# Kernel optimization log

Measured on AMD Instinct MI355X. Metric: run time of the kernel, lower is better.

## Reference

```python
import jax, jax.numpy as jnp
import numpy as np


def setup_inputs() -> dict:
    key = jax.random.key(0)
    k1, k2, k3 = jax.random.split(key, 3)
    B, T, I, H, D = 32, 1024, 1024, 16, 64
    x = jax.random.normal(k1, (B, T, I), dtype=jnp.float32)
    kv_kernel = jax.random.normal(k2, (I, H, D, 2), dtype=jnp.float32) * (1.0 / np.sqrt(I))
    q_kernel = jax.random.normal(k3, (H, D), dtype=jnp.float32) * (1.0 / np.sqrt(D))
    return {"x": x, "kv_kernel": kv_kernel, "q_kernel": q_kernel}


def _attention_rnn(x, kv_kernel, q_kernel):
    # x: [B,T,I]; kv_kernel: [I,H,D,2]; q_kernel: [H,D]
    B, T, _ = x.shape
    H, D = q_kernel.shape
    # Projection + silu activation, done once for all timesteps (same math as per-step einsum)
    kv = jnp.einsum('bti,ihdk->bthdk', x, kv_kernel)
    kv = jax.nn.silu(kv)
    k = kv[..., 0]  # [B,T,H,D]
    v = kv[..., 1]  # [B,T,H,D]
    # Per-step attention score s_t = <q_h, k_th>
    s = jnp.einsum('hd,bthd->bth', q_kernel, k)  # [B,T,H]

    # Keras RNN zero-initialized states: num [B,H,D], den [B,H], max [B,H]
    init = (
        jnp.zeros((B, H, D), x.dtype),
        jnp.zeros((B, H), x.dtype),
        jnp.zeros((B, H), x.dtype),
    )

    def step(carry, inp):
        num, den, pmax = carry
        s_t, v_t = inp  # [B,H], [B,H,D]
        cmax = jnp.maximum(pmax, s_t)
        exp_max_diff = jnp.exp(pmax - cmax)
        sm = jnp.exp(s_t - cmax)
        den_n = sm + den * exp_max_diff
        num_n = v_t * sm[..., None] + num * exp_max_diff[..., None]
        h = num_n / den_n[..., None]          # [B,H,D]
        o = jnp.sum(h, axis=-2)               # concat_heads=False -> sum over heads: [B,D]
        return (num_n, den_n, cmax), o

    # scan over time (leading axis)
    _, outs = jax.lax.scan(step, init, (jnp.swapaxes(s, 0, 1), jnp.swapaxes(v, 0, 1)))
    return jnp.swapaxes(outs, 0, 1)  # [B,T,D]


def reference(x, kv_kernel, q_kernel):
    return _attention_rnn(x, kv_kernel, q_kernel)
```

## Files before the change

### kernel.cpp

```cpp
#include <hip/hip_runtime.h>
#include <hip/hip_bf16.h>

#define B_ 32
#define T_ 1024
#define H_ 16
#define D_ 64
#define M_ (B_*T_)
#define N_ (H_*D_*2)
#define K_ 1024
#define CHUNKS 16
#define CLEN (T_/CHUNKS)

typedef __bf16 bf16x8 __attribute__((ext_vector_type(8)));
typedef float  f32x4  __attribute__((ext_vector_type(4)));
typedef unsigned short u16x8 __attribute__((ext_vector_type(8)));

__device__ __forceinline__ float bf2f(unsigned short u){
  union{ float f; unsigned int i; } c; c.i = ((unsigned int)u) << 16; return c.f;
}
__device__ __forceinline__ unsigned short f2bf(float f){
  union{ float f; unsigned int i; } c; c.f = f;
  unsigned int r = (c.i + 0x7FFFu + ((c.i >> 16) & 1u)) >> 16;
  return (unsigned short)r;
}
__device__ __forceinline__ float silu(float x){ return x / (1.0f + __expf(-x)); }

__device__ __forceinline__ void gload16(const void* g, void* l){
  __builtin_amdgcn_global_load_lds(
      (const __attribute__((address_space(1))) void*)g,
      (__attribute__((address_space(3))) void*)l, 16, 0, 0);
}

#define BAR()   __builtin_amdgcn_s_barrier()
#define LGKM0() asm volatile("s_waitcnt lgkmcnt(0)" ::: "memory")
#define VM4()   asm volatile("s_waitcnt vmcnt(4)" ::: "memory")
#define VM0()   asm volatile("s_waitcnt vmcnt(0)" ::: "memory")

__global__ __launch_bounds__(256) void cvt_x(const float* __restrict__ x,
                                             unsigned short* __restrict__ xb, int n){
  int i = (blockIdx.x * 256 + threadIdx.x) * 8;
  int stride = gridDim.x * 256 * 8;
  for(; i < n; i += stride){
    float4 v0 = *(const float4*)(x + i);
    float4 v1 = *(const float4*)(x + i + 4);
    u16x8 o;
    o[0]=f2bf(v0.x); o[1]=f2bf(v0.y); o[2]=f2bf(v0.z); o[3]=f2bf(v0.w);
    o[4]=f2bf(v1.x); o[5]=f2bf(v1.y); o[6]=f2bf(v1.z); o[7]=f2bf(v1.w);
    *(u16x8*)(xb + i) = o;
  }
}

__global__ __launch_bounds__(256) void cvt_w(const float* __restrict__ w,
                                             unsigned short* __restrict__ wt){
  __shared__ unsigned short tile[64][65];
  int kt = blockIdx.x * 64, nt = blockIdx.y * 64;
  int t = threadIdx.x, tn = t & 63, tk4 = t >> 6;
  #pragma unroll
  for(int r = 0; r < 16; ++r){
    int kl = r * 4 + tk4;
    tile[tn][kl] = f2bf(w[(kt + kl) * N_ + nt + tn]);
  }
  __syncthreads();
  #pragma unroll
  for(int r = 0; r < 16; ++r){
    int nl = r * 4 + tk4;
    int n  = nt + nl;
    int np = (n & ~127) | ((n & 1) << 6) | ((n >> 1) & 63);
    wt[(size_t)np * K_ + kt + tn] = tile[nl][tn];
  }
}

__global__ __launch_bounds__(512, 2) void gemm8(
    const unsigned short* __restrict__ xb,
    const unsigned short* __restrict__ wt,
    const float*  __restrict__ q,
    unsigned short* __restrict__ vout,
    float* __restrict__ s)
{
  __shared__ __align__(16) char lds[131072];

  const int t = threadIdx.x, lane = t & 63, wid = t >> 6;
  const int wr = wid >> 2, wc = wid & 3;
  const int l15 = lane & 15, l4 = lane >> 4;

  const int id  = blockIdx.y * gridDim.x + blockIdx.x;
  const int swz = (id & 7) * 128 + (id >> 3);
  const int bx = swz & 127, by = swz >> 7;
  const int brow = bx * 256, bcol = by * 256;

  f32x4 acc[8][4] = {};
  bf16x8 af[8], b0[4], b1[4];

  const int swl   = l15 & 7;
  const int aoff0 = l15 * 128 + (((0 + l4) ^ swl) << 4);
  const int aoff1 = l15 * 128 + (((4 + l4) ^ swl) << 4);

  auto stage = [&](int buf, int op, int half, const unsigned short* src,
                   int rowbase, int kt){
    char* base = lds + buf * 65536 + op * 32768 + half * 16384;
    #pragma unroll
    for(int L = 0; L < 2; ++L){
      int idx = L * 512 + t;
      int r = idx >> 3, ss = idx & 7;
      gload16(src + (size_t)(rowbase + half * 128 + r) * K_
                  + kt * 64 + ((ss ^ (r & 7)) << 3),
              base + idx * 16);
    }
  };
  auto rdA = [&](int buf, int miBase){
    const char* base = lds + buf * 65536 + wr * 16384;
    #pragma unroll
    for(int m = 0; m < 4; ++m){
      af[m*2+0] = *(const bf16x8*)(base + (miBase + m) * 2048 + aoff0);
      af[m*2+1] = *(const bf16x8*)(base + (miBase + m) * 2048 + aoff1);
    }
  };
  auto rdB = [&](int buf, int niBase, bf16x8 (&dst)[4]){
    const char* base = lds + buf * 65536 + 32768 + (wc >> 1) * 16384 + (wc & 1) * 8192;
    #pragma unroll
    for(int n = 0; n < 2; ++n){
      dst[n*2+0] = *(const bf16x8*)(base + (niBase + n) * 2048 + aoff0);
      dst[n*2+1] = *(const bf16x8*)(base + (niBase + n) * 2048 + aoff1);
    }
  };
  auto mmaq = [&](int miBase, bf16x8 (&bb)[4], int niBase){
    __builtin_amdgcn_s_setprio(1);
    #pragma unroll
    for(int m = 0; m < 4; ++m)
      #pragma unroll
      for(int n = 0; n < 2; ++n)
        #pragma unroll
        for(int k = 0; k < 2; ++k)
          acc[miBase+m][niBase+n] = __builtin_amdgcn_mfma_f32_16x16x32_bf16(
              af[m*2+k], bb[n*2+k], acc[miBase+m][niBase+n], 0, 0, 0);
    __builtin_amdgcn_s_setprio(0);
  };

  stage(0,0,0, xb, brow, 0); stage(0,0,1, xb, brow, 0);
  stage(0,1,0, wt, bcol, 0); stage(0,1,1, wt, bcol, 0);
  stage(1,1,0, wt, bcol, 1); stage(1,1,1, wt, bcol, 1);
  VM4(); BAR();

  for(int i = 0; i < 7; ++i){
    const int t1 = 2*i + 1;
    const int t2 = 2*i + 2;
    const int t3 = 2*i + 3;
    rdA(0,0); rdB(0,0,b0); stage(1,0,0, xb, brow, t1);
    BAR(); LGKM0(); mmaq(0,b0,0); BAR();
    rdB(0,2,b1); stage(1,0,1, xb, brow, t1);
    BAR(); LGKM0(); mmaq(0,b1,2); BAR();
    rdA(0,4); stage(0,1,0, wt, bcol, t2);
    BAR(); LGKM0(); mmaq(4,b1,2); BAR();
    stage(0,1,1, wt, bcol, t2); VM4();
    BAR(); mmaq(4,b0,0); BAR();
    rdA(1,0); rdB(1,0,b0); stage(0,0,0, xb, brow, t2);
    BAR(); LGKM0(); mmaq(0,b0,0); BAR();
    rdB(1,2,b1); stage(0,0,1, xb, brow, t2);
    BAR(); LGKM0(); mmaq(0,b1,2); BAR();
    rdA(1,4); stage(1,1,0, wt, bcol, t3);
    BAR(); LGKM0(); mmaq(4,b1,2); BAR();
    stage(1,1,1, wt, bcol, t3); VM4();
    BAR(); mmaq(4,b0,0); BAR();
  }
  rdA(0,0); rdB(0,0,b0); stage(1,0,0, xb, brow, 15);
  BAR(); LGKM0(); mmaq(0,b0,0); BAR();
  rdB(0,2,b1); stage(1,0,1, xb, brow, 15);
  BAR(); LGKM0(); mmaq(0,b1,2); BAR();
  rdA(0,4);
  BAR(); LGKM0(); mmaq(4,b1,2); BAR();
  VM0();
  BAR(); mmaq(4,b0,0); BAR();
  rdA(1,0); rdB(1,0,b0);
  BAR(); LGKM0(); mmaq(0,b0,0); BAR();
  rdB(1,2,b1);
  BAR(); LGKM0(); mmaq(0,b1,2); BAR();
  rdA(1,4);
  BAR(); LGKM0(); mmaq(4,b1,2); BAR();
  mmaq(4,b0,0);

  const int hh = by * 2 + (wc >> 1);
  if(wc & 1){
    #pragma unroll
    for(int mi = 0; mi < 8; ++mi)
      #pragma unroll
      for(int r = 0; r < 4; ++r){
        const int gm = brow + wr*128 + mi*16 + l4*4 + r;
        const int bb = gm >> 10, tt = gm & (T_-1);
        unsigned short* vrow = vout + (((size_t)bb*H_ + hh)*T_ + tt)*D_;
        #pragma unroll
        for(int ni = 0; ni < 4; ++ni)
          vrow[ni*16 + l15] = f2bf(silu(acc[mi][ni][r]));
      }
  } else {
    float qv[4];
    #pragma unroll
    for(int ni = 0; ni < 4; ++ni) qv[ni] = q[hh*D_ + ni*16 + l15];
    #pragma unroll
    for(int mi = 0; mi < 8; ++mi)
      #pragma unroll
      for(int r = 0; r < 4; ++r){
        float sc = 0.f;
        #pragma unroll
        for(int ni = 0; ni < 4; ++ni) sc += qv[ni] * silu(acc[mi][ni][r]);
        sc += __shfl_xor(sc, 1); sc += __shfl_xor(sc, 2);
        sc += __shfl_xor(sc, 4); sc += __shfl_xor(sc, 8);
        if(l15 == 0){
          const int gm = brow + wr*128 + mi*16 + l4*4 + r;
          s[(size_t)gm * H_ + hh] = sc;
        }
      }
  }
}

__global__ __launch_bounds__(256) void scan1(
    const unsigned short* __restrict__ v, const float* __restrict__ s,
    float* __restrict__ snum, float* __restrict__ sden, float* __restrict__ smax)
{
  __shared__ float sst[CLEN][H_+1];
  const int blk = blockIdx.x;
  const int c = blk & (CHUNKS-1), b = blk / CHUNKS;
  const int t = threadIdx.x, lane = t & 63, w = t >> 6, h0 = w * 4;

  const float* sbase = s + ((size_t)b*T_ + c*CLEN) * H_;
  for(int i = t; i < CLEN*H_; i += 256) sst[i >> 4][i & 15] = sbase[i];
  __syncthreads();

  float mfix[4];
  #pragma unroll
  for(int j = 0; j < 4; ++j){
    float mm = sst[lane][h0 + j];
    mm = fmaxf(mm, __shfl_xor(mm, 1));  mm = fmaxf(mm, __shfl_xor(mm, 2));
    mm = fmaxf(mm, __shfl_xor(mm, 4));  mm = fmaxf(mm, __shfl_xor(mm, 8));
    mm = fmaxf(mm, __shfl_xor(mm, 16)); mm = fmaxf(mm, __shfl_xor(mm, 32));
    mfix[j] = mm;
  }

  float den[4] = {0.f,0.f,0.f,0.f}, num[4] = {0.f,0.f,0.f,0.f};
  const unsigned short* vb = v + (((size_t)b*H_ + h0)*T_ + c*CLEN)*D_;
  for(int tt = 0; tt < CLEN; ++tt){
    #pragma unroll
    for(int j = 0; j < 4; ++j){
      float p  = __expf(sst[tt][h0 + j] - mfix[j]);
      float vt = bf2f(vb[(size_t)j*T_*D_ + tt*D_ + lane]);
      den[j] += p;
      num[j] += p * vt;
    }
  }
  #pragma unroll
  for(int j = 0; j < 4; ++j){
    int sb = (b*H_ + h0 + j)*CHUNKS + c;
    snum[(size_t)sb*64 + lane] = num[j];
    if(lane == 0){ sden[sb] = den[j]; smax[sb] = mfix[j]; }
  }
}

__global__ __launch_bounds__(256) void scan2h(
    const unsigned short* __restrict__ v, const float* __restrict__ s,
    const float* __restrict__ snum, const float* __restrict__ sden,
    const float* __restrict__ smax, float* __restrict__ out)
{
  __shared__ float sst[CLEN][H_+1];
  __shared__ float oacc[4][CLEN][68];
  const int blk = blockIdx.x;
  const int c = blk & (CHUNKS-1), b = blk / CHUNKS;
  const int t = threadIdx.x, lane = t & 63, w = t >> 6, h0 = w * 4;

  const float* sbase = s + ((size_t)b*T_ + c*CLEN) * H_;
  for(int i = t; i < CLEN*H_; i += 256) sst[i >> 4][i & 15] = sbase[i];
  __syncthreads();

  float num[4], den[4], m[4];
  #pragma unroll
  for(int j = 0; j < 4; ++j){ num[j] = 0.f; den[j] = 0.f; m[j] = -3.0e38f; }

  for(int cc = 0; cc < c; ++cc){
    #pragma unroll
    for(int j = 0; j < 4; ++j){
      int sb = (b*H_ + h0 + j)*CHUNKS + cc;
      float m2 = smax[sb], d2 = sden[sb], n2 = snum[(size_t)sb*64 + lane];
      float cm = fmaxf(m[j], m2);
      float e1 = __expf(m[j]-cm), e2 = __expf(m2-cm);
      den[j] = den[j]*e1 + d2*e2;
      num[j] = num[j]*e1 + n2*e2;
      m[j] = cm;
    }
  }

  float mfix[4];
  #pragma unroll
  for(int j = 0; j < 4; ++j){
    int sb = (b*H_ + h0 + j)*CHUNKS + c;
    mfix[j] = fmaxf(m[j], smax[sb]);
    float sc = __expf(m[j] - mfix[j]);
    den[j] *= sc;
    num[j] *= sc;
  }

  const unsigned short* vb = v + (((size_t)b*H_ + h0)*T_ + c*CLEN)*D_;
  for(int tt = 0; tt < CLEN; ++tt){
    float o = 0.f;
    #pragma unroll
    for(int j = 0; j < 4; ++j){
      float p  = __expf(sst[tt][h0 + j] - mfix[j]);
      float vt = bf2f(vb[(size_t)j*T_*D_ + tt*D_ + lane]);
      den[j] += p;
      num[j] += p * vt;
      o += num[j] / den[j];
    }
    oacc[w][tt][lane] = o;
  }
  __syncthreads();

  {
    int tt = t >> 2, db = (t & 3) * 16;
    float* ob = out + ((size_t)b*T_ + c*CLEN + tt) * D_ + db;
    #pragma unroll
    for(int qd = 0; qd < 4; ++qd){
      f32x4 a0 = *(const f32x4*)&oacc[0][tt][db + qd*4];
      f32x4 a1 = *(const f32x4*)&oacc[1][tt][db + qd*4];
      f32x4 a2 = *(const f32x4*)&oacc[2][tt][db + qd*4];
      f32x4 a3 = *(const f32x4*)&oacc[3][tt][db + qd*4];
      f32x4 r = (a0 + a1) + (a2 + a3);
      *(f32x4*)(ob + qd*4) = r;
    }
  }
}

extern "C" void kernel_launch(void* const* d_in, const int* in_sizes, int n_in,
                              void* d_out, int out_size, void* d_ws, size_t ws_size,
                              hipStream_t stream){
  (void)in_sizes; (void)n_in; (void)out_size; (void)ws_size;
  const float* x = (const float*)d_in[0];
  const float* w = (const float*)d_in[1];
  const float* q = (const float*)d_in[2];
  float* out = (float*)d_out;
  char* ws = (char*)d_ws;

  unsigned short* wt   = (unsigned short*)(ws);
  unsigned short* xb   = (unsigned short*)(ws + (4u  << 20));
  unsigned short* vbuf = (unsigned short*)(ws + (68u << 20));
  float* s    = (float*)(ws + (132u << 20));
  float* snum = (float*)(ws + (8u  << 20));
  float* sden = (float*)(ws + (12u << 20));
  float* smax = (float*)(ws + (12u << 20) + (1u << 16));

  cvt_x<<<2048, 256, 0, stream>>>(x, xb, M_ * K_);
  cvt_w<<<dim3(K_/64, N_/64), 256, 0, stream>>>(w, wt);
  gemm8<<<dim3(M_/256, N_/256), 512, 0, stream>>>(xb, wt, q, vbuf, s);
  scan1<<<B_*CHUNKS, 256, 0, stream>>>(vbuf, s, snum, sden, smax);
  scan2h<<<B_*CHUNKS, 256, 0, stream>>>(vbuf, s, snum, sden, smax, out);
}
```

Baseline: 253.5 us.

## Fuse chunk-scan first pass into GEMM epilogue and merge conversion kernels

Moves the per-chunk max, denominator and weighted-numerator computation of the first scan pass into the GEMM epilogue. Softmax weights go through LDS from the score warps to the value warps, which removes the scan1 kernel and its re-read of the bf16 V buffer. It also merges the x and weight fp32-to-bf16 conversion kernels into one launch. The cost is extra barriers and epilogue work inside the GEMM, plus LDS reuse after the main loop.

Result: slower. 277.0 us (+9.3%).

```diff
diff --git a/kernel.cpp b/kernel.cpp
--- a/kernel.cpp
+++ b/kernel.cpp
@@ -36,37 +36,40 @@
 #define VM4()   asm volatile("s_waitcnt vmcnt(4)" ::: "memory")
 #define VM0()   asm volatile("s_waitcnt vmcnt(0)" ::: "memory")
 
-__global__ __launch_bounds__(256) void cvt_x(const float* __restrict__ x,
-                                             unsigned short* __restrict__ xb, int n){
-  int i = (blockIdx.x * 256 + threadIdx.x) * 8;
-  int stride = gridDim.x * 256 * 8;
-  for(; i < n; i += stride){
-    float4 v0 = *(const float4*)(x + i);
-    float4 v1 = *(const float4*)(x + i + 4);
-    u16x8 o;
-    o[0]=f2bf(v0.x); o[1]=f2bf(v0.y); o[2]=f2bf(v0.z); o[3]=f2bf(v0.w);
-    o[4]=f2bf(v1.x); o[5]=f2bf(v1.y); o[6]=f2bf(v1.z); o[7]=f2bf(v1.w);
-    *(u16x8*)(xb + i) = o;
-  }
-}
-
-__global__ __launch_bounds__(256) void cvt_w(const float* __restrict__ w,
-                                             unsigned short* __restrict__ wt){
+__global__ __launch_bounds__(256) void cvt_xw(const float* __restrict__ x,
+                                              unsigned short* __restrict__ xb,
+                                              const float* __restrict__ w,
+                                              unsigned short* __restrict__ wt){
   __shared__ unsigned short tile[64][65];
-  int kt = blockIdx.x * 64, nt = blockIdx.y * 64;
-  int t = threadIdx.x, tn = t & 63, tk4 = t >> 6;
-  #pragma unroll
-  for(int r = 0; r < 16; ++r){
-    int kl = r * 4 + tk4;
-    tile[tn][kl] = f2bf(w[(kt + kl) * N_ + nt + tn]);
-  }
-  __syncthreads();
-  #pragma unroll
-  for(int r = 0; r < 16; ++r){
-    int nl = r * 4 + tk4;
-    int n  = nt + nl;
-    int np = (n & ~127) | ((n & 1) << 6) | ((n >> 1) & 63);
-    wt[(size_t)np * K_ + kt + tn] = tile[nl][tn];
+  if(blockIdx.x < 2048){
+    int i = (blockIdx.x * 256 + threadIdx.x) * 8;
+    int stride = 2048 * 256 * 8;
+    int n = M_ * K_;
+    for(; i < n; i += stride){
+      float4 v0 = *(const float4*)(x + i);
+      float4 v1 = *(const float4*)(x + i + 4);
+      u16x8 o;
+      o[0]=f2bf(v0.x); o[1]=f2bf(v0.y); o[2]=f2bf(v0.z); o[3]=f2bf(v0.w);
+      o[4]=f2bf(v1.x); o[5]=f2bf(v1.y); o[6]=f2bf(v1.z); o[7]=f2bf(v1.w);
+      *(u16x8*)(xb + i) = o;
+    }
+  } else {
+    int blk = blockIdx.x - 2048;
+    int kt = (blk & 15) * 64, nt = (blk >> 4) * 64;
+    int t = threadIdx.x, tn = t & 63, tk4 = t >> 6;
+    #pragma unroll
+    for(int r = 0; r < 16; ++r){
+      int kl = r * 4 + tk4;
+      tile[tn][kl] = f2bf(w[(kt + kl) * N_ + nt + tn]);
+    }
+    __syncthreads();
+    #pragma unroll
+    for(int r = 0; r < 16; ++r){
+      int nl = r * 4 + tk4;
+      int n  = nt + nl;
+      int np = (n & ~127) | ((n & 1) << 6) | ((n >> 1) & 63);
+      wt[(size_t)np * K_ + kt + tn] = tile[nl][tn];
+    }
   }
 }
 
@@ -75,7 +78,10 @@
     const unsigned short* __restrict__ wt,
     const float*  __restrict__ q,
     unsigned short* __restrict__ vout,
-    float* __restrict__ s)
+    float* __restrict__ s,
+    float* __restrict__ snum,
+    float* __restrict__ sden,
+    float* __restrict__ smax)
 {
   __shared__ __align__(16) char lds[131072];
 
@@ -178,79 +184,83 @@
   BAR(); LGKM0(); mmaq(4,b1,2); BAR();
   mmaq(4,b0,0);
 
-  const int hh = by * 2 + (wc >> 1);
+  __syncthreads();
+  float* plds = (float*)lds;
+  const int hl = wc >> 1;
+  const int hh = by * 2 + hl;
+  const int b  = brow >> 10;
+  const int c0 = (brow & (T_-1)) >> 6;
+
+  if(!(wc & 1)){
+    float qv[4];
+    #pragma unroll
+    for(int ni = 0; ni < 4; ++ni) qv[ni] = q[hh*D_ + ni*16 + l15];
+    float sc[8][4];
+    #pragma unroll
+    for(int mi = 0; mi < 8; ++mi)
+      #pragma unroll
+      for(int r = 0; r < 4; ++r){
+        float v = 0.f;
+        #pragma unroll
+        for(int ni = 0; ni < 4; ++ni) v += qv[ni] * silu(acc[mi][ni][r]);
+        v += __shfl_xor(v, 1); v += __shfl_xor(v, 2);
+        v += __shfl_xor(v, 4); v += __shfl_xor(v, 8);
+        sc[mi][r] = v;
+        if(l15 == 0)
+          s[(size_t)(brow + wr*128 + mi*16 + l4*4 + r) * H_ + hh] = v;
+      }
+    #pragma unroll
+    for(int ch = 0; ch < 2; ++ch){
+      float mm = -3.0e38f;
+      #pragma unroll
+      for(int mj = 0; mj < 4; ++mj)
+        #pragma unroll
+        for(int r = 0; r < 4; ++r) mm = fmaxf(mm, sc[ch*4+mj][r]);
+      mm = fmaxf(mm, __shfl_xor(mm, 16));
+      mm = fmaxf(mm, __shfl_xor(mm, 32));
+      float dd = 0.f;
+      #pragma unroll
+      for(int mj = 0; mj < 4; ++mj)
+        #pragma unroll
+        for(int r = 0; r < 4; ++r){
+          float p = __expf(sc[ch*4+mj][r] - mm);
+          dd += p;
+          if(l15 == 0)
+            plds[hl*256 + wr*128 + (ch*4+mj)*16 + l4*4 + r] = p;
+        }
+      dd += __shfl_xor(dd, 16); dd += __shfl_xor(dd, 32);
+      const int sb = (b*H_ + hh)*CHUNKS + c0 + wr*2 + ch;
+      if(lane == 0){ sden[sb] = dd; smax[sb] = mm; }
+    }
+  }
+  __syncthreads();
   if(wc & 1){
+    float nm[2][4] = {{0.f,0.f,0.f,0.f},{0.f,0.f,0.f,0.f}};
     #pragma unroll
     for(int mi = 0; mi < 8; ++mi)
       #pragma unroll
       for(int r = 0; r < 4; ++r){
-        const int gm = brow + wr*128 + mi*16 + l4*4 + r;
-        const int bb = gm >> 10, tt = gm & (T_-1);
-        unsigned short* vrow = vout + (((size_t)bb*H_ + hh)*T_ + tt)*D_;
-        #pragma unroll
-        for(int ni = 0; ni < 4; ++ni)
-          vrow[ni*16 + l15] = f2bf(silu(acc[mi][ni][r]));
-      }
-  } else {
-    float qv[4];
-    #pragma unroll
-    for(int ni = 0; ni < 4; ++ni) qv[ni] = q[hh*D_ + ni*16 + l15];
-    #pragma unroll
-    for(int mi = 0; mi < 8; ++mi)
-      #pragma unroll
-      for(int r = 0; r < 4; ++r){
-        float sc = 0.f;
-        #pragma unroll
-        for(int ni = 0; ni < 4; ++ni) sc += qv[ni] * silu(acc[mi][ni][r]);
-        sc += __shfl_xor(sc, 1); sc += __shfl_xor(sc, 2);
-        sc += __shfl_xor(sc, 4); sc += __shfl_xor(sc, 8);
-        if(l15 == 0){
-          const int gm = brow + wr*128 + mi*16 + l4*4 + r;
-          s[(size_t)gm * H_ + hh] = sc;
+        const int lrow = wr*128 + mi*16 + l4*4 + r;
+        const int tt = (brow + lrow) & (T_-1);
+        unsigned short* vrow = vout + (((size_t)b*H_ + hh)*T_ + tt)*D_;
+        const float p = plds[hl*256 + lrow];
+        #pragma unroll
+        for(int ni = 0; ni < 4; ++ni){
+          float sv = silu(acc[mi][ni][r]);
+          vrow[ni*16 + l15] = f2bf(sv);
+          nm[mi>>2][ni] += p * sv;
         }
       }
-  }
-}
-
-__global__ __launch_bounds__(256) void scan1(
-    const unsigned short* __restrict__ v, const float* __restrict__ s,
-    float* __restrict__ snum, float* __restrict__ sden, float* __restrict__ smax)
-{
-  __shared__ float sst[CLEN][H_+1];
-  const int blk = blockIdx.x;
-  const int c = blk & (CHUNKS-1), b = blk / CHUNKS;
-  const int t = threadIdx.x, lane = t & 63, w = t >> 6, h0 = w * 4;
-
-  const float* sbase = s + ((size_t)b*T_ + c*CLEN) * H_;
-  for(int i = t; i < CLEN*H_; i += 256) sst[i >> 4][i & 15] = sbase[i];
-  __syncthreads();
-
-  float mfix[4];
-  #pragma unroll
-  for(int j = 0; j < 4; ++j){
-    float mm = sst[lane][h0 + j];
-    mm = fmaxf(mm, __shfl_xor(mm, 1));  mm = fmaxf(mm, __shfl_xor(mm, 2));
-    mm = fmaxf(mm, __shfl_xor(mm, 4));  mm = fmaxf(mm, __shfl_xor(mm, 8));
-    mm = fmaxf(mm, __shfl_xor(mm, 16)); mm = fmaxf(mm, __shfl_xor(mm, 32));
-    mfix[j] = mm;
-  }
-
-  float den[4] = {0.f,0.f,0.f,0.f}, num[4] = {0.f,0.f,0.f,0.f};
-  const unsigned short* vb = v + (((size_t)b*H_ + h0)*T_ + c*CLEN)*D_;
-  for(int tt = 0; tt < CLEN; ++tt){
-    #pragma unroll
-    for(int j = 0; j < 4; ++j){
-      float p  = __expf(sst[tt][h0 + j] - mfix[j]);
-      float vt = bf2f(vb[(size_t)j*T_*D_ + tt*D_ + lane]);
-      den[j] += p;
-      num[j] += p * vt;
-    }
-  }
-  #pragma unroll
-  for(int j = 0; j < 4; ++j){
-    int sb = (b*H_ + h0 + j)*CHUNKS + c;
-    snum[(size_t)sb*64 + lane] = num[j];
-    if(lane == 0){ sden[sb] = den[j]; smax[sb] = mfix[j]; }
+    #pragma unroll
+    for(int ch = 0; ch < 2; ++ch){
+      const int sb = (b*H_ + hh)*CHUNKS + c0 + wr*2 + ch;
+      #pragma unroll
+      for(int ni = 0; ni < 4; ++ni){
+        float nmv = nm[ch][ni];
+        nmv += __shfl_xor(nmv, 16); nmv += __shfl_xor(nmv, 32);
+        if(l4 == 0) snum[(size_t)sb*64 + ni*16 + l15] = nmv;
+      }
+    }
   }
 }
 
@@ -340,13 +350,12 @@
   unsigned short* xb   = (unsigned short*)(ws + (4u  << 20));
   unsigned short* vbuf = (unsigned short*)(ws + (68u << 20));
   float* s    = (float*)(ws + (132u << 20));
-  float* snum = (float*)(ws + (8u  << 20));
-  float* sden = (float*)(ws + (12u << 20));
-  float* smax = (float*)(ws + (12u << 20) + (1u << 16));
-
-  cvt_x<<<2048, 256, 0, stream>>>(x, xb, M_ * K_);
-  cvt_w<<<dim3(K_/64, N_/64), 256, 0, stream>>>(w, wt);
-  gemm8<<<dim3(M_/256, N_/256), 512, 0, stream>>>(xb, wt, q, vbuf, s);
-  scan1<<<B_*CHUNKS, 256, 0, stream>>>(vbuf, s, snum, sden, smax);
+  float* snum = (float*)(ws + (134u << 20));
+  float* sden = (float*)(ws + (136u << 20));
+  float* smax = (float*)(ws + (136u << 20) + (1u << 16));
+
+  cvt_xw<<<2048 + 512, 256, 0, stream>>>(x, xb, w, wt);
+  gemm8<<<dim3(M_/256, N_/256), 512, 0, stream>>>(xb, wt, q, vbuf, s,
+                                                  snum, sden, smax);
   scan2h<<<B_*CHUNKS, 256, 0, stream>>>(vbuf, s, snum, sden, smax, out);
 }
```
